# Kernel optimization log

Hardware: AMD Instinct MI355X
Metric: run time of the kernel (lower is better)

The kernel has to match this reference:

```python
import jax, jax.numpy as jnp
import numpy as np

NODES_PER_GRAPH = 128


def _leaky(x):
    return jnp.where(x >= 0, x, 0.01 * x)


def _graph_conv(x, W, src, dst, w_e, n_nodes):
    # DGL GraphConv, norm='both', bias=False, with edge_weight.
    # Structural (unweighted) degrees, clamped to 1, as in DGL.
    ones = jnp.ones(src.shape[0], dtype=x.dtype)
    deg_out = jnp.clip(jax.ops.segment_sum(ones, src, num_segments=n_nodes), 1.0)
    deg_in = jnp.clip(jax.ops.segment_sum(ones, dst, num_segments=n_nodes), 1.0)
    x = x * (deg_out ** -0.5)[:, None]
    if W.shape[0] > W.shape[1]:  # in_feats > out_feats: project first (DGL order)
        x = x @ W
    msg = x[src] * w_e[:, None]                     # [E, d]
    agg = jax.ops.segment_sum(msg, dst, num_segments=n_nodes)
    agg = agg * (deg_in ** -0.5)[:, None]
    if W.shape[0] <= W.shape[1]:
        agg = agg @ W
    return agg


def setup_inputs() -> dict:
    key = jax.random.key(0)
    ks = jax.random.split(key, 8)
    N, E = 131072, 1048576
    in_feats, hidden, readout = 64, 256, 128
    return {
        "node_feats": jax.random.normal(ks[0], (N, in_feats), dtype=jnp.float32),
        "edge_weight": jax.random.uniform(ks[1], (E,), dtype=jnp.float32),
        "W1": jax.random.normal(ks[2], (in_feats, hidden), dtype=jnp.float32) * 0.1,
        "W2": jax.random.normal(ks[3], (hidden, readout), dtype=jnp.float32) * 0.05,
        "W_lin": jax.random.normal(ks[4], (readout, 64), dtype=jnp.float32) * 0.1,
        "W_cls": jax.random.normal(ks[5], (64, 16), dtype=jnp.float32) * 0.1,
        "edge_src": jax.random.randint(ks[6], (E,), 0, N, dtype=jnp.int32),
        "edge_dst": jax.random.randint(ks[7], (E,), 0, N, dtype=jnp.int32),
    }


def reference(node_feats, edge_weight, W1, W2, W_lin, W_cls, edge_src, edge_dst):
    N = node_feats.shape[0]
    G = N // NODES_PER_GRAPH
    h = _leaky(_graph_conv(node_feats, W1, edge_src, edge_dst, edge_weight, N))
    h = _leaky(_graph_conv(h, W2, edge_src, edge_dst, edge_weight, N))
    # mean_nodes readout over batched graphs of equal size
    gid = jnp.arange(N, dtype=jnp.int32) // NODES_PER_GRAPH
    pooled = jax.ops.segment_sum(h, gid, num_segments=G) / NODES_PER_GRAPH
    # linear -> dropout(eval: identity) -> classifier (no activation in head)
    return (pooled @ W_lin) @ W_cls
```

## Files before the change

kernel.cpp:

```cpp
#include <hip/hip_runtime.h>


constexpr int NPG = 128;
constexpr int F0  = 64;
constexpr int F1  = 256;
constexpr int F2  = 128;
constexpr int BMM = 64;
constexpr int H2  = 136;
constexpr int CAP = 40;
constexpr int NXCD = 8;

using bf16x8 = __attribute__((ext_vector_type(8))) short;
using f32x4  = __attribute__((ext_vector_type(4))) float;
using u16x8  = __attribute__((ext_vector_type(8))) unsigned short;

__device__ __forceinline__ float leaky(float x) {
    return (x >= 0.f) ? x : 0.01f * x;
}

__device__ __forceinline__ unsigned short f2bf(float x) {
    unsigned u = __float_as_uint(x);
    return (unsigned short)((u + 0x7FFFu + ((u >> 16) & 1u)) >> 16);
}
__device__ __forceinline__ float bf2f(unsigned short h) {
    return __uint_as_float(((unsigned)h) << 16);
}
__device__ __forceinline__ void split2(float x, unsigned short& hi, unsigned short& lo) {
    hi = f2bf(x);
    lo = f2bf(x - bf2f(hi));
}

__device__ __forceinline__ f32x4 mfma16(bf16x8 a, bf16x8 b, f32x4 c) {
    return __builtin_amdgcn_mfma_f32_16x16x32_bf16(a, b, c, 0, 0, 0);
}

__device__ __forceinline__ unsigned get_xcc() {
    unsigned xcc;
    asm("s_getreg_b32 %0, hwreg(HW_REG_XCC_ID)" : "=s"(xcc));
    return xcc & (NXCD - 1);
}


__global__ void k_count_fill(const int* __restrict__ src, const int* __restrict__ dst,
                             const float* __restrict__ we,
                             int* __restrict__ cnt_priv,
                             int* __restrict__ cnt_dst,
                             long long* __restrict__ slots, unsigned E, int N) {
    const unsigned xcc = get_xcc();
    unsigned e = blockIdx.x * 256u + threadIdx.x;
    if (e < E) {
        const int s = src[e], d = dst[e];
        const int pos = atomicAdd(&cnt_dst[d], 1);
        if (pos < CAP) {
            const long long v = ((long long)(unsigned)__float_as_int(we[e]) << 32)
                              | (unsigned)s;
            __builtin_nontemporal_store(v, &slots[(size_t)d * CAP + pos]);
        }
        __hip_atomic_fetch_add(&cnt_priv[(size_t)xcc * N + s], 1,
                               __ATOMIC_RELAXED, __HIP_MEMORY_SCOPE_WORKGROUP);
    }
}

__global__ void k_finalize_deg(const int* __restrict__ cnt_priv,
                               const int* __restrict__ cnt_dst,
                               float* __restrict__ dinv_out, float* __restrict__ dinv_in,
                               int N) {
    int i = blockIdx.x * blockDim.x + threadIdx.x;
    if (i < N) {
        int c = 0;
#pragma unroll
        for (int x = 0; x < NXCD; ++x) c += cnt_priv[(size_t)x * N + i];
        dinv_out[i] = rsqrtf((float)max(c, 1));
        dinv_in[i]  = rsqrtf((float)max(cnt_dst[i], 1));
    }
}

__global__ void __launch_bounds__(256) k_scale_w(
        int2* __restrict__ slots, const int* __restrict__ cnt_dst,
        const float* __restrict__ dinv_out, int N) {
    int gid = blockIdx.x * 256 + threadIdx.x;
    int n = gid >> 3;
    int j0 = gid & 7;
    if (n >= N) return;
    const int cnt = min(cnt_dst[n], CAP);
    for (int j = j0; j < cnt; j += 8) {
        const size_t idx = (size_t)n * CAP + j;
        int2 p = slots[idx];
        p.y = __float_as_int(__int_as_float(p.y) * dinv_out[p.x]);
        slots[idx] = p;
    }
}

__global__ void __launch_bounds__(256) k_feats_bf(
        const float4* __restrict__ in, u16x8* __restrict__ out, int total8) {
    int gid = blockIdx.x * 256 + threadIdx.x;
    if (gid < total8) {
        const float4 v0 = in[gid * 2];
        const float4 v1 = in[gid * 2 + 1];
        u16x8 r;
        r[0] = f2bf(v0.x); r[1] = f2bf(v0.y); r[2] = f2bf(v0.z); r[3] = f2bf(v0.w);
        r[4] = f2bf(v1.x); r[5] = f2bf(v1.y); r[6] = f2bf(v1.z); r[7] = f2bf(v1.w);
        out[gid] = r;
    }
}

__global__ void k_wsplit1(const float* __restrict__ W1,
                          unsigned short* __restrict__ w1h, unsigned short* __restrict__ w1l) {
    int i = blockIdx.x * 256 + threadIdx.x;
    if (i < F1 * F0) {
        int n = i >> 6, k = i & 63;
        unsigned short h, l;
        split2(W1[k * F1 + n], h, l);
        w1h[i] = h; w1l[i] = l;
    }
}
__global__ void k_wsplit2(const float* __restrict__ W2,
                          unsigned short* __restrict__ w2h, unsigned short* __restrict__ w2l) {
    int i = blockIdx.x * 256 + threadIdx.x;
    if (i < F2 * F1) {
        int n = i >> 8, k = i & 255;
        unsigned short h, l;
        split2(W2[k * F2 + n], h, l);
        w2h[i] = h; w2l[i] = l;
    }
}

__global__ void __launch_bounds__(256) k_gather1(
        const u16x8* __restrict__ featsb,
        const int* __restrict__ cnt_dst,
        const int2* __restrict__ slots, const float* __restrict__ dinv_in,
        unsigned short* __restrict__ a1h, unsigned short* __restrict__ a1l, int N) {
    const int gid = blockIdx.x * 256 + threadIdx.x;
    const int n = gid >> 3;
    const int s = gid & 7;
    if (n >= N) return;
    const size_t b = (size_t)n * CAP;
    const int cnt = min(cnt_dst[n], CAP);
    float a[8];
#pragma unroll
    for (int k = 0; k < 8; ++k) a[k] = 0.f;
    int j = 0;
    for (; j + 4 <= cnt; j += 4) {
        const int2 p0 = slots[b + j], p1 = slots[b + j + 1];
        const int2 p2 = slots[b + j + 2], p3 = slots[b + j + 3];
        const u16x8 u0 = featsb[(size_t)p0.x * 8 + s];
        const u16x8 u1 = featsb[(size_t)p1.x * 8 + s];
        const u16x8 u2 = featsb[(size_t)p2.x * 8 + s];
        const u16x8 u3 = featsb[(size_t)p3.x * 8 + s];
        const float w0 = __int_as_float(p0.y), w1 = __int_as_float(p1.y);
        const float w2 = __int_as_float(p2.y), w3 = __int_as_float(p3.y);
#pragma unroll
        for (int k = 0; k < 8; ++k) {
            a[k] = fmaf(bf2f(u0[k]), w0, a[k]);
            a[k] = fmaf(bf2f(u1[k]), w1, a[k]);
            a[k] = fmaf(bf2f(u2[k]), w2, a[k]);
            a[k] = fmaf(bf2f(u3[k]), w3, a[k]);
        }
    }
    for (; j < cnt; ++j) {
        const int2 p = slots[b + j];
        const u16x8 u = featsb[(size_t)p.x * 8 + s];
        const float w = __int_as_float(p.y);
#pragma unroll
        for (int k = 0; k < 8; ++k) a[k] = fmaf(bf2f(u[k]), w, a[k]);
    }
    const float din = dinv_in[n];
    u16x8 hv, lv;
#pragma unroll
    for (int k = 0; k < 8; ++k) {
        unsigned short h, l;
        split2(a[k] * din, h, l);
        hv[k] = h; lv[k] = l;
    }
    const size_t off = (size_t)n * 8 + s;
    ((u16x8*)a1h)[off] = hv;
    ((u16x8*)a1l)[off] = lv;
}

__global__ void __launch_bounds__(256, 4) k_mfma_fused(
        const unsigned short* __restrict__ a1h, const unsigned short* __restrict__ a1l,
        const unsigned short* __restrict__ w1h, const unsigned short* __restrict__ w1l,
        const unsigned short* __restrict__ w2h, const unsigned short* __restrict__ w2l,
        unsigned short* __restrict__ x2b) {
    __shared__ unsigned short hhi[BMM][H2];
    __shared__ unsigned short hlo[BMM][H2];
    const int tid  = threadIdx.x;
    const int w    = tid >> 6;
    const int lane = tid & 63;
    const int r    = lane & 15;
    const int kg   = lane >> 4;
    const int base = blockIdx.x * BMM;

    f32x4 acc1[4][4] = {};
#pragma unroll
    for (int ks = 0; ks < 2; ++ks) {
        const int kk = ks * 32 + kg * 8;
        bf16x8 wh[4], wl[4];
#pragma unroll
        for (int j = 0; j < 4; ++j) {
            const int col = (j >> 1) * 128 + w * 32 + (j & 1) * 16 + r;
            wh[j] = *(const bf16x8*)(w1h + col * F0 + kk);
            wl[j] = *(const bf16x8*)(w1l + col * F0 + kk);
        }
#pragma unroll
        for (int mt = 0; mt < 4; ++mt) {
            const size_t aoff = (size_t)(base + mt * 16 + r) * F0 + kk;
            const bf16x8 ah = *(const bf16x8*)(a1h + aoff);
            const bf16x8 al = *(const bf16x8*)(a1l + aoff);
#pragma unroll
            for (int j = 0; j < 4; ++j) {
                acc1[mt][j] = mfma16(ah, wh[j], acc1[mt][j]);
                acc1[mt][j] = mfma16(ah, wl[j], acc1[mt][j]);
                acc1[mt][j] = mfma16(al, wh[j], acc1[mt][j]);
            }
        }
    }

    f32x4 acc2[4][2] = {};
    const int c2base = w * 32;
#pragma unroll
    for (int h = 0; h < 2; ++h) {
#pragma unroll
        for (int jn = 0; jn < 2; ++jn) {
            const int j = h * 2 + jn;
            const int lc = w * 32 + jn * 16 + r;
#pragma unroll
            for (int mt = 0; mt < 4; ++mt)
#pragma unroll
                for (int i = 0; i < 4; ++i) {
                    const int rl = mt * 16 + kg * 4 + i;
                    unsigned short hi_, lo_;
                    split2(leaky(acc1[mt][j][i]), hi_, lo_);
                    hhi[rl][lc] = hi_;
                    hlo[rl][lc] = lo_;
                }
        }
        __syncthreads();
#pragma unroll
        for (int ks = 0; ks < 4; ++ks) {
            const int lkk = ks * 32 + kg * 8;
            const int kglob = h * 128 + lkk;
            bf16x8 w2hv[2], w2lv[2];
#pragma unroll
            for (int nt = 0; nt < 2; ++nt) {
                const int col = c2base + nt * 16 + r;
                w2hv[nt] = *(const bf16x8*)(w2h + col * F1 + kglob);
                w2lv[nt] = *(const bf16x8*)(w2l + col * F1 + kglob);
            }
#pragma unroll
            for (int mt = 0; mt < 4; ++mt) {
                const int rl = mt * 16 + r;
                const bf16x8 ah = *(const bf16x8*)&hhi[rl][lkk];
                const bf16x8 al = *(const bf16x8*)&hlo[rl][lkk];
#pragma unroll
                for (int nt = 0; nt < 2; ++nt) {
                    acc2[mt][nt] = mfma16(ah, w2hv[nt], acc2[mt][nt]);
                    acc2[mt][nt] = mfma16(ah, w2lv[nt], acc2[mt][nt]);
                    acc2[mt][nt] = mfma16(al, w2hv[nt], acc2[mt][nt]);
                }
            }
        }
        __syncthreads();
    }

#pragma unroll
    for (int mt = 0; mt < 4; ++mt)
#pragma unroll
        for (int nt = 0; nt < 2; ++nt)
#pragma unroll
            for (int i = 0; i < 4; ++i) {
                const int row = base + mt * 16 + kg * 4 + i;
                const int col = c2base + nt * 16 + r;
                x2b[(size_t)row * F2 + col] = f2bf(acc2[mt][nt][i]);
            }
}

__global__ void __launch_bounds__(256) k_gather2_pool4(
        const ushort* __restrict__ x2b, const int* __restrict__ cnt_dst,
        const int2* __restrict__ slots, const float* __restrict__ dinv_in,
        float* __restrict__ pooled) {
    const int g = blockIdx.x >> 2;
    const int c = blockIdx.x & 3;
    const int t = threadIdx.x;
    const int q = t >> 2;
    const int s = t & 3;
    const int d8 = c * 4 + s;
    const u16x8* x2v = (const u16x8*)x2b;

    float pool[8];
#pragma unroll
    for (int k = 0; k < 8; ++k) pool[k] = 0.f;
    const int nbase = g * NPG;

#pragma unroll
    for (int i = 0; i < NPG; i += 64) {
        const int n = nbase + i + q;
        const size_t b = (size_t)n * CAP;
        const int cnt = min(cnt_dst[n], CAP);
        float a[8];
#pragma unroll
        for (int k = 0; k < 8; ++k) a[k] = 0.f;
        int j = 0;
        for (; j + 4 <= cnt; j += 4) {
            const int2 p0 = slots[b + j], p1 = slots[b + j + 1];
            const int2 p2 = slots[b + j + 2], p3 = slots[b + j + 3];
            const u16x8 u0 = x2v[(size_t)p0.x * 16 + d8];
            const u16x8 u1 = x2v[(size_t)p1.x * 16 + d8];
            const u16x8 u2 = x2v[(size_t)p2.x * 16 + d8];
            const u16x8 u3 = x2v[(size_t)p3.x * 16 + d8];
            const float w0 = __int_as_float(p0.y), w1 = __int_as_float(p1.y);
            const float w2 = __int_as_float(p2.y), w3 = __int_as_float(p3.y);
#pragma unroll
            for (int k = 0; k < 8; ++k) {
                a[k] = fmaf(bf2f(u0[k]), w0, a[k]);
                a[k] = fmaf(bf2f(u1[k]), w1, a[k]);
                a[k] = fmaf(bf2f(u2[k]), w2, a[k]);
                a[k] = fmaf(bf2f(u3[k]), w3, a[k]);
            }
        }
        for (; j < cnt; ++j) {
            const int2 p = slots[b + j];
            const float w = __int_as_float(p.y);
            const u16x8 u = x2v[(size_t)p.x * 16 + d8];
#pragma unroll
            for (int k = 0; k < 8; ++k) a[k] = fmaf(bf2f(u[k]), w, a[k]);
        }
        const float din = dinv_in[n];
#pragma unroll
        for (int k = 0; k < 8; ++k) pool[k] += leaky(a[k] * din);
    }

    __shared__ float pl[64][4][9];
#pragma unroll
    for (int k = 0; k < 8; ++k) pl[q][s][k] = pool[k];
    __syncthreads();
#pragma unroll
    for (int off = 32; off >= 1; off >>= 1) {
        if (q < off) {
#pragma unroll
            for (int k = 0; k < 8; ++k) {
                pool[k] += pl[q + off][s][k];
                pl[q][s][k] = pool[k];
            }
        }
        __syncthreads();
    }
    if (q == 0) {
        const float inv = 1.0f / NPG;
        float* dstp = pooled + (size_t)g * F2 + c * 32 + s * 8;
#pragma unroll
        for (int k = 0; k < 8; ++k) dstp[k] = pool[k] * inv;
    }
}

__global__ void __launch_bounds__(64) k_head(
        const float* __restrict__ pooled,
        const float* __restrict__ Wlin,
        const float* __restrict__ Wcls,
        float* __restrict__ out) {
    const int g = blockIdx.x;
    const int t = threadIdx.x;
    __shared__ float p[F2];
    __shared__ float tj[64];
    p[t]      = pooled[(size_t)g * F2 + t];
    p[t + 64] = pooled[(size_t)g * F2 + 64 + t];
    __syncthreads();
    float s = 0.f;
#pragma unroll
    for (int k = 0; k < F2; ++k) s = fmaf(p[k], Wlin[k * 64 + t], s);
    tj[t] = s;
    __syncthreads();
    if (t < 16) {
        float sum = 0.f;
#pragma unroll
        for (int j = 0; j < 64; ++j) sum = fmaf(tj[j], Wcls[j * 16 + t], sum);
        out[g * 16 + t] = sum;
    }
}

extern "C" void kernel_launch(void* const* d_in, const int* in_sizes, int n_in,
                              void* d_out, int out_size, void* d_ws, size_t ws_size,
                              hipStream_t stream) {
    const float* feats = (const float*)d_in[0];
    const float* we    = (const float*)d_in[1];
    const float* W1    = (const float*)d_in[2];
    const float* W2    = (const float*)d_in[3];
    const float* Wlin  = (const float*)d_in[4];
    const float* Wcls  = (const float*)d_in[5];
    const int*   src   = (const int*)d_in[6];
    const int*   dst   = (const int*)d_in[7];

    const int N = in_sizes[0] / F0;
    const unsigned E = (unsigned)in_sizes[1];
    const int G = N / NPG;

    float* out = (float*)d_out;

    int* ws_i = (int*)d_ws;
    size_t o = 0;
    auto align4 = [&]() { o = (o + 3) & ~(size_t)3; };
    int* cnt_dst = ws_i + o; o += N;
    int* cnt_priv = ws_i + o; o += (size_t)NXCD * N;
    float* dinv_out = (float*)(ws_i + o); o += N;
    float* dinv_in  = (float*)(ws_i + o); o += N;
    align4();
    int2* slots = (int2*)(ws_i + o); o += 2 * (size_t)N * CAP;
    unsigned short* featsb = (unsigned short*)(ws_i + o); o += (size_t)N * 32;
    unsigned short* a1h = (unsigned short*)(ws_i + o); o += (size_t)N * 32;
    unsigned short* a1l = (unsigned short*)(ws_i + o); o += (size_t)N * 32;
    unsigned short* x2b = (unsigned short*)(ws_i + o); o += (size_t)N * 64;
    unsigned short* w1h = (unsigned short*)(ws_i + o); o += (F1 * F0) / 2;
    unsigned short* w1l = (unsigned short*)(ws_i + o); o += (F1 * F0) / 2;
    unsigned short* w2h = (unsigned short*)(ws_i + o); o += (F2 * F1) / 2;
    unsigned short* w2l = (unsigned short*)(ws_i + o); o += (F2 * F1) / 2;
    align4();
    float* pooled = (float*)(ws_i + o); o += (size_t)G * F2;

    hipMemsetAsync(cnt_dst, 0, (size_t)(1 + NXCD) * N * sizeof(int), stream);

    k_count_fill<<<(E + 255) / 256, 256, 0, stream>>>(
        src, dst, we, cnt_priv, cnt_dst, (long long*)slots, E, N);

    k_finalize_deg<<<(N + 255) / 256, 256, 0, stream>>>(
        cnt_priv, cnt_dst, dinv_out, dinv_in, N);

    k_scale_w<<<(N * 8 + 255) / 256, 256, 0, stream>>>(slots, cnt_dst, dinv_out, N);

    k_feats_bf<<<(N * 8 + 255) / 256, 256, 0, stream>>>(
        (const float4*)feats, (u16x8*)featsb, N * 8);

    k_wsplit1<<<(F1 * F0 + 255) / 256, 256, 0, stream>>>(W1, w1h, w1l);
    k_wsplit2<<<(F2 * F1 + 255) / 256, 256, 0, stream>>>(W2, w2h, w2l);

    k_gather1<<<(N * 8 + 255) / 256, 256, 0, stream>>>(
        (const u16x8*)featsb, cnt_dst, slots, dinv_in, a1h, a1l, N);

    k_mfma_fused<<<N / BMM, 256, 0, stream>>>(a1h, a1l, w1h, w1l, w2h, w2l, x2b);

    k_gather2_pool4<<<G * 4, 256, 0, stream>>>(
        x2b, cnt_dst, slots, dinv_in, pooled);
    k_head<<<G, 64, 0, stream>>>(pooled, Wlin, Wcls, out);
}
```

Measured before the change: 315.9 us.

## Fold source-degree normalization into node features and drop edge-weight scaling pass

Removes the k_scale_w pass that rescaled every CSR slot weight by dinv_out[src]. Instead, dinv_out is applied per node: to the input features before bf16 conversion, and to the layer-2 projected rows in the MFMA epilogue. The feature conversion and both weight-split kernels are merged into one k_prep launch with block-range dispatch. This avoids a random-gather read-modify-write over the slot array and three launches, at the cost of a few extra multiplies and slightly different bf16 rounding points.

```diff
diff --git a/kernel.cpp b/kernel.cpp
--- a/kernel.cpp
+++ b/kernel.cpp
@@ -75,50 +75,36 @@
     }
 }
 
-__global__ void __launch_bounds__(256) k_scale_w(
-        int2* __restrict__ slots, const int* __restrict__ cnt_dst,
-        const float* __restrict__ dinv_out, int N) {
-    int gid = blockIdx.x * 256 + threadIdx.x;
-    int n = gid >> 3;
-    int j0 = gid & 7;
-    if (n >= N) return;
-    const int cnt = min(cnt_dst[n], CAP);
-    for (int j = j0; j < cnt; j += 8) {
-        const size_t idx = (size_t)n * CAP + j;
-        int2 p = slots[idx];
-        p.y = __float_as_int(__int_as_float(p.y) * dinv_out[p.x]);
-        slots[idx] = p;
-    }
-}
-
-__global__ void __launch_bounds__(256) k_feats_bf(
-        const float4* __restrict__ in, u16x8* __restrict__ out, int total8) {
-    int gid = blockIdx.x * 256 + threadIdx.x;
-    if (gid < total8) {
-        const float4 v0 = in[gid * 2];
-        const float4 v1 = in[gid * 2 + 1];
+__global__ void __launch_bounds__(256) k_prep(
+        const float4* __restrict__ featsv, const float* __restrict__ dinv_out,
+        u16x8* __restrict__ featsb,
+        const float* __restrict__ W1,
+        unsigned short* __restrict__ w1h, unsigned short* __restrict__ w1l,
+        const float* __restrict__ W2,
+        unsigned short* __restrict__ w2h, unsigned short* __restrict__ w2l,
+        int N) {
+    const int nfb = N >> 5;
+    const int b = blockIdx.x;
+    if (b < nfb) {
+        const int gid = b * 256 + threadIdx.x;
+        const float4 v0 = featsv[gid * 2];
+        const float4 v1 = featsv[gid * 2 + 1];
+        const float d = dinv_out[gid >> 3];
         u16x8 r;
-        r[0] = f2bf(v0.x); r[1] = f2bf(v0.y); r[2] = f2bf(v0.z); r[3] = f2bf(v0.w);
-        r[4] = f2bf(v1.x); r[5] = f2bf(v1.y); r[6] = f2bf(v1.z); r[7] = f2bf(v1.w);
-        out[gid] = r;
-    }
-}
-
-__global__ void k_wsplit1(const float* __restrict__ W1,
-                          unsigned short* __restrict__ w1h, unsigned short* __restrict__ w1l) {
-    int i = blockIdx.x * 256 + threadIdx.x;
-    if (i < F1 * F0) {
-        int n = i >> 6, k = i & 63;
+        r[0] = f2bf(v0.x * d); r[1] = f2bf(v0.y * d);
+        r[2] = f2bf(v0.z * d); r[3] = f2bf(v0.w * d);
+        r[4] = f2bf(v1.x * d); r[5] = f2bf(v1.y * d);
+        r[6] = f2bf(v1.z * d); r[7] = f2bf(v1.w * d);
+        featsb[gid] = r;
+    } else if (b < nfb + 64) {
+        const int i = (b - nfb) * 256 + threadIdx.x;
+        const int n = i >> 6, k = i & 63;
         unsigned short h, l;
         split2(W1[k * F1 + n], h, l);
         w1h[i] = h; w1l[i] = l;
-    }
-}
-__global__ void k_wsplit2(const float* __restrict__ W2,
-                          unsigned short* __restrict__ w2h, unsigned short* __restrict__ w2l) {
-    int i = blockIdx.x * 256 + threadIdx.x;
-    if (i < F2 * F1) {
-        int n = i >> 8, k = i & 255;
+    } else {
+        const int i = (b - nfb - 64) * 256 + threadIdx.x;
+        const int n = i >> 8, k = i & 255;
         unsigned short h, l;
         split2(W2[k * F2 + n], h, l);
         w2h[i] = h; w2l[i] = l;
@@ -181,6 +167,7 @@
         const unsigned short* __restrict__ a1h, const unsigned short* __restrict__ a1l,
         const unsigned short* __restrict__ w1h, const unsigned short* __restrict__ w1l,
         const unsigned short* __restrict__ w2h, const unsigned short* __restrict__ w2l,
+        const float* __restrict__ dinv_out,
         unsigned short* __restrict__ x2b) {
     __shared__ unsigned short hhi[BMM][H2];
     __shared__ unsigned short hlo[BMM][H2];
@@ -266,13 +253,15 @@
 #pragma unroll
     for (int mt = 0; mt < 4; ++mt)
 #pragma unroll
-        for (int nt = 0; nt < 2; ++nt)
-#pragma unroll
-            for (int i = 0; i < 4; ++i) {
-                const int row = base + mt * 16 + kg * 4 + i;
+        for (int i = 0; i < 4; ++i) {
+            const int row = base + mt * 16 + kg * 4 + i;
+            const float dsc = dinv_out[row];
+#pragma unroll
+            for (int nt = 0; nt < 2; ++nt) {
                 const int col = c2base + nt * 16 + r;
-                x2b[(size_t)row * F2 + col] = f2bf(acc2[mt][nt][i]);
-            }
+                x2b[(size_t)row * F2 + col] = f2bf(acc2[mt][nt][i] * dsc);
+            }
+        }
 }
 
 __global__ void __launch_bounds__(256) k_gather2_pool4(
@@ -424,18 +413,15 @@
     k_finalize_deg<<<(N + 255) / 256, 256, 0, stream>>>(
         cnt_priv, cnt_dst, dinv_out, dinv_in, N);
 
-    k_scale_w<<<(N * 8 + 255) / 256, 256, 0, stream>>>(slots, cnt_dst, dinv_out, N);
-
-    k_feats_bf<<<(N * 8 + 255) / 256, 256, 0, stream>>>(
-        (const float4*)feats, (u16x8*)featsb, N * 8);
-
-    k_wsplit1<<<(F1 * F0 + 255) / 256, 256, 0, stream>>>(W1, w1h, w1l);
-    k_wsplit2<<<(F2 * F1 + 255) / 256, 256, 0, stream>>>(W2, w2h, w2l);
+    k_prep<<<(N >> 5) + 64 + 128, 256, 0, stream>>>(
+        (const float4*)feats, dinv_out, (u16x8*)featsb,
+        W1, w1h, w1l, W2, w2h, w2l, N);
 
     k_gather1<<<(N * 8 + 255) / 256, 256, 0, stream>>>(
         (const u16x8*)featsb, cnt_dst, slots, dinv_in, a1h, a1l, N);
 
-    k_mfma_fused<<<N / BMM, 256, 0, stream>>>(a1h, a1l, w1h, w1l, w2h, w2l, x2b);
+    k_mfma_fused<<<N / BMM, 256, 0, stream>>>(
+        a1h, a1l, w1h, w1l, w2h, w2l, dinv_out, x2b);
 
     k_gather2_pool4<<<G * 4, 256, 0, stream>>>(
         x2b, cnt_dst, slots, dinv_in, pooled);
```

Result: faster. 298.0 us (-5.7%).
